# Optimization experiments

Measured on AMD Instinct MI355X. Metric: run time of the kernel, lower is better.

## Reference

```python
import jax, jax.numpy as jnp
import numpy as np

N, F_IN, HID, H1, NG = 50000, 128, 64, 4, 512
E = 800000


def setup_inputs() -> dict:
    key = jax.random.key(0)
    ks = jax.random.split(key, 16)
    x = jax.random.normal(ks[0], (N, F_IN), dtype=jnp.float32)
    edge_index = jax.random.randint(ks[1], (2, E), 0, N, dtype=jnp.int64)
    batch = jnp.sort(jax.random.randint(ks[2], (N,), 0, NG, dtype=jnp.int64))
    s = 0.05
    W1 = jax.random.normal(ks[3], (F_IN, H1 * HID), dtype=jnp.float32) * s
    a_src1 = jax.random.normal(ks[4], (H1, HID), dtype=jnp.float32) * s
    a_dst1 = jax.random.normal(ks[5], (H1, HID), dtype=jnp.float32) * s
    b1 = jnp.zeros((H1 * HID,), dtype=jnp.float32)
    W2 = jax.random.normal(ks[6], (H1 * HID, HID), dtype=jnp.float32) * s
    a_src2 = jax.random.normal(ks[7], (1, HID), dtype=jnp.float32) * s
    a_dst2 = jax.random.normal(ks[8], (1, HID), dtype=jnp.float32) * s
    b2 = jnp.zeros((HID,), dtype=jnp.float32)
    Wc = jax.random.normal(ks[9], (HID, 2), dtype=jnp.float32) * s
    bc = jnp.zeros((2,), dtype=jnp.float32)
    return dict(x=x, edge_index=edge_index, batch=batch, W1=W1, a_src1=a_src1,
                a_dst1=a_dst1, b1=b1, W2=W2, a_src2=a_src2, a_dst2=a_dst2,
                b2=b2, Wc=Wc, bc=bc)


def gat_layer(x, W, a_src, a_dst, bias, src, dst, n):
    # PyG GATConv: h = x @ W per head; e_ij = LeakyReLU(a_src.h_j + a_dst.h_i),
    # softmax over incoming edges of each dst node, then scatter-add aggregate.
    H, D = a_src.shape
    h = (x @ W).reshape(n, H, D)                       # [N,H,D]
    asrc = jnp.einsum('nhd,hd->nh', h, a_src)          # [N,H]
    adst = jnp.einsum('nhd,hd->nh', h, a_dst)
    e = jax.nn.leaky_relu(asrc[src] + adst[dst], 0.2)  # [E,H]
    m = jax.lax.stop_gradient(jax.ops.segment_max(e, dst, num_segments=n))
    p = jnp.exp(e - m[dst])
    s = jax.ops.segment_sum(p, dst, num_segments=n)
    alpha = p / (s[dst] + 1e-16)                       # [E,H]
    out = jax.ops.segment_sum(alpha[:, :, None] * h[src], dst, num_segments=n)
    return out.reshape(n, H * D) + bias


def reference(x, edge_index, batch, W1, a_src1, a_dst1, b1, W2, a_src2, a_dst2, b2, Wc, bc):
    n = x.shape[0]
    loops = jnp.arange(n, dtype=edge_index.dtype)
    src = jnp.concatenate([edge_index[0], loops])  # add self-loops (PyG default)
    dst = jnp.concatenate([edge_index[1], loops])
    h = jax.nn.relu(gat_layer(x, W1, a_src1, a_dst1, b1, src, dst, n))
    h = jax.nn.relu(gat_layer(h, W2, a_src2, a_dst2, b2, src, dst, n))
    # global mean pool over graphs
    ng = NG
    sums = jax.ops.segment_sum(h, batch, num_segments=ng)
    cnts = jax.ops.segment_sum(jnp.ones((n,), h.dtype), batch, num_segments=ng)
    pooled = sums / jnp.maximum(cnts, 1.0)[:, None]
    logits = pooled @ Wc + bc
    return jax.nn.log_softmax(logits, axis=1)
```

## Files before the change

kernel.cpp:

```cpp
#include <hip/hip_runtime.h>
#include <hip/hip_bf16.h>
#include <cstddef>
#include <cstdint>

#define FIN   128
#define HID   64
#define H1    4
#define NGRAPH 512
#define BCAP  8192

typedef short bf16x8 __attribute__((ext_vector_type(8)));
typedef float f32x4  __attribute__((ext_vector_type(4)));
typedef float f32x2  __attribute__((ext_vector_type(2)));

#if defined(__has_builtin)
#if __has_builtin(__builtin_amdgcn_cvt_f32_fp8) && __has_builtin(__builtin_amdgcn_cvt_pk_fp8_f32)
#define HAVE_HW_FP8 1
#endif
#if __has_builtin(__builtin_amdgcn_cvt_pk_f32_fp8)
#define HAVE_HW_FP8_PK 1
#endif
#endif

__device__ __forceinline__ float wave_reduce_sum(float v) {
  #pragma unroll
  for (int off = 32; off > 0; off >>= 1) v += __shfl_down(v, off, 64);
  return v;
}

__device__ __forceinline__ float leaky02(float x) {
  return x > 0.0f ? x : 0.2f * x;
}

__device__ __forceinline__ float bf2f(unsigned short u) {
  union { unsigned int i; float f; } v; v.i = ((unsigned int)u) << 16; return v.f;
}
__device__ __forceinline__ unsigned short f2bf(float f) {
  union { float f; unsigned int i; } v; v.f = f;
  unsigned int b = v.i;
  return (unsigned short)((b + 0x7FFFu + ((b >> 16) & 1u)) >> 16);
}

#ifndef HAVE_HW_FP8
__device__ __forceinline__ unsigned char f2fp8_1(float f) {
  unsigned int u = __float_as_uint(f);
  unsigned int s = u >> 31;
  u &= 0x7fffffffu;
  if (u > 0x43e00000u) u = 0x43e00000u;
  unsigned int b = u + (0x0007FFFFu + ((u >> 20) & 1u));
  int e = (int)(b >> 23) - 127;
  unsigned int m = (b >> 20) & 7u;
  unsigned char o;
  if (e < -9) o = 0;
  else if (e < -6) { int sh = -6 - e; o = (unsigned char)((8u | m) >> sh); }
  else if (e > 8) o = 0x7e;
  else o = (unsigned char)(((e + 7) << 3) | m);
  return o | (unsigned char)(s << 7);
}
#endif
__device__ __forceinline__ float fp8tof_1(unsigned char b) {
  unsigned int s = b >> 7, e = (b >> 3) & 15u, m = b & 7u;
  float v = (e == 0) ? (float)m * 0.001953125f
                     : (float)(8u + m) * __uint_as_float((117u + e) << 23);
  return s ? -v : v;
}

__device__ __forceinline__ unsigned char f2fp8(float f) {
#ifdef HAVE_HW_FP8
  return (unsigned char)(__builtin_amdgcn_cvt_pk_fp8_f32(f, f, 0u, false) & 0xffu);
#else
  return f2fp8_1(f);
#endif
}

__device__ __forceinline__ void fma4_fp8(unsigned int hw, float p,
                                         float& a0, float& a1, float& a2, float& a3) {
#ifdef HAVE_HW_FP8_PK
  f32x2 lo = __builtin_amdgcn_cvt_pk_f32_fp8((int)hw, false);
  f32x2 hi = __builtin_amdgcn_cvt_pk_f32_fp8((int)hw, true);
  a0 = fmaf(p, lo.x, a0);
  a1 = fmaf(p, lo.y, a1);
  a2 = fmaf(p, hi.x, a2);
  a3 = fmaf(p, hi.y, a3);
#elif defined(HAVE_HW_FP8)
  a0 = fmaf(p, __builtin_amdgcn_cvt_f32_fp8(hw, 0), a0);
  a1 = fmaf(p, __builtin_amdgcn_cvt_f32_fp8(hw, 1), a1);
  a2 = fmaf(p, __builtin_amdgcn_cvt_f32_fp8(hw, 2), a2);
  a3 = fmaf(p, __builtin_amdgcn_cvt_f32_fp8(hw, 3), a3);
#else
  a0 = fmaf(p, fp8tof_1((unsigned char)(hw & 0xffu)), a0);
  a1 = fmaf(p, fp8tof_1((unsigned char)((hw >> 8) & 0xffu)), a1);
  a2 = fmaf(p, fp8tof_1((unsigned char)((hw >> 16) & 0xffu)), a2);
  a3 = fmaf(p, fp8tof_1((unsigned char)((hw >> 24) & 0xffu)), a3);
#endif
}

#define P3K 8
__global__ __launch_bounds__(256)
void bpart_kernel(const int* __restrict__ src, const int* __restrict__ dst,
                  int* __restrict__ bucketFill, unsigned int* __restrict__ bucketBuf,
                  const float* __restrict__ W1, const float* __restrict__ W2,
                  unsigned short* __restrict__ W1T, unsigned short* __restrict__ W2T,
                  const int* __restrict__ batch, int* __restrict__ gstart,
                  int* __restrict__ gend, int E, int N, int nbuck) {
  int tid = threadIdx.x;
  int stride = gridDim.x * 256;
  int t0 = blockIdx.x * 256 + tid;
  for (int u = t0; u < 256 * 128; u += stride) {
    int n = u >> 7, k = u & 127;
    W1T[u] = f2bf(W1[(size_t)k * 256 + n]);
  }
  for (int u = t0; u < 64 * 256; u += stride) {
    int n = u >> 8, k = u & 255;
    W2T[u] = f2bf(W2[(size_t)k * 64 + n]);
  }
  for (int i = t0; i < N; i += stride) {
    int g = batch[i];
    if (i == 0 || batch[i - 1] != g) gstart[g] = i;
    if (i == N - 1 || batch[i + 1] != g) gend[g] = i + 1;
  }

  __shared__ int lhist[256];
  __shared__ int lbase[256];
  int chunk = 256 * P3K;
  for (int start = blockIdx.x * chunk; start < E; start += gridDim.x * chunk) {
    lhist[tid] = 0;
    __syncthreads();
    int mybuck[P3K]; unsigned int mypack[P3K]; int myrank[P3K];
    #pragma unroll
    for (int k = 0; k < P3K; k++) {
      int i = start + k * 256 + tid;
      if (i < E) {
        int d = dst[i];
        int b = d >> 8;
        mybuck[k] = b;
        mypack[k] = (unsigned int)src[i] | ((unsigned int)(d & 255) << 16);
        myrank[k] = atomicAdd(&lhist[b], 1);
      } else mybuck[k] = -1;
    }
    __syncthreads();
    if (tid < nbuck) lbase[tid] = (lhist[tid] > 0) ? atomicAdd(&bucketFill[tid], lhist[tid]) : 0;
    __syncthreads();
    #pragma unroll
    for (int k = 0; k < P3K; k++) {
      if (mybuck[k] >= 0) {
        int b = mybuck[k];
        int pos = lbase[b] + myrank[k];
        if (pos < BCAP) bucketBuf[((size_t)b << 13) + pos] = mypack[k];
      }
    }
    __syncthreads();
  }
}

__global__ __launch_bounds__(256)
void bbuild_gemm1_kernel(const unsigned int* __restrict__ bucketBuf,
                         const int* __restrict__ bucketFill,
                         int* __restrict__ rowstart, int* __restrict__ rowend,
                         unsigned short* __restrict__ csr,
                         const float* __restrict__ X, const unsigned short* __restrict__ W1T,
                         unsigned char* __restrict__ h1f8,
                         const float* __restrict__ a_src, const float* __restrict__ a_dst,
                         float* __restrict__ asv, float* __restrict__ adv,
                         int N, int nbuck) {
  __shared__ union {
    struct { unsigned short As[64][136]; unsigned short Bs[256][40]; } g;
    struct { int ldeg[256]; int lscan[256]; int lfill[256]; } b;
  } sm;
  int tid = threadIdx.x;

  if (blockIdx.x < (unsigned)nbuck) {
    int b = blockIdx.x;
    int r0 = b << 13;
    int cnt = bucketFill[b]; if (cnt > BCAP) cnt = BCAP;
    int nb0 = b << 8;
    sm.b.ldeg[tid] = 0;
    __syncthreads();
    for (int j = tid; j < cnt; j += 256)
      atomicAdd(&sm.b.ldeg[bucketBuf[r0 + j] >> 16], 1);
    __syncthreads();
    int v = sm.b.ldeg[tid];
    sm.b.lscan[tid] = v;
    __syncthreads();
    for (int off = 1; off < 256; off <<= 1) {
      int u = (tid >= off) ? sm.b.lscan[tid - off] : 0;
      __syncthreads();
      sm.b.lscan[tid] += u;
      __syncthreads();
    }
    int excl = sm.b.lscan[tid] - v;
    sm.b.lfill[tid] = excl;
    if (nb0 + tid < N) {
      rowstart[nb0 + tid] = r0 + excl;
      rowend[nb0 + tid]   = r0 + excl + v;
    }
    __syncthreads();
    for (int j = tid; j < cnt; j += 256) {
      unsigned int p = bucketBuf[r0 + j];
      int pos = r0 + atomicAdd(&sm.b.lfill[p >> 16], 1);
      csr[pos] = (unsigned short)(p & 0xffffu);
    }
    return;
  }

  int t = tid;
  int w = t >> 6, lane = t & 63;
  int quad = lane >> 4, l16 = lane & 15;
  int blockRow = (blockIdx.x - nbuck) * 64;

  {
    int node = t >> 2, kp = (t & 3) * 32;
    int gn = blockRow + node; if (gn >= N) gn = N - 1;
    const float4* xp = (const float4*)(X + (size_t)gn * 128 + kp);
    #pragma unroll
    for (int i = 0; i < 4; i++) {
      float4 va = xp[2 * i], vb = xp[2 * i + 1];
      union { unsigned short u[8]; uint4 v; } r;
      r.u[0] = f2bf(va.x); r.u[1] = f2bf(va.y); r.u[2] = f2bf(va.z); r.u[3] = f2bf(va.w);
      r.u[4] = f2bf(vb.x); r.u[5] = f2bf(vb.y); r.u[6] = f2bf(vb.z); r.u[7] = f2bf(vb.w);
      *(uint4*)&sm.g.As[node][kp + i * 8] = r.v;
    }
  }

  f32x4 acc[4][4];
  #pragma unroll
  for (int i = 0; i < 4; i++)
    #pragma unroll
    for (int j = 0; j < 4; j++) acc[i][j] = (f32x4){0.f, 0.f, 0.f, 0.f};

  for (int kc = 0; kc < FIN; kc += 32) {
    {
      const unsigned short* wp = W1T + (size_t)t * 128 + kc;
      #pragma unroll
      for (int i = 0; i < 4; i++) {
        uint4 v = *(const uint4*)(wp + i * 8);
        *(uint4*)&sm.g.Bs[t][i * 8] = v;
      }
    }
    __syncthreads();
    bf16x8 af[4], bfr[4];
    #pragma unroll
    for (int mt = 0; mt < 4; mt++)
      af[mt] = *(const bf16x8*)&sm.g.As[mt * 16 + l16][kc + quad * 8];
    #pragma unroll
    for (int nt = 0; nt < 4; nt++)
      bfr[nt] = *(const bf16x8*)&sm.g.Bs[w * 64 + nt * 16 + l16][quad * 8];
    #pragma unroll
    for (int mt = 0; mt < 4; mt++)
      #pragma unroll
      for (int nt = 0; nt < 4; nt++)
        acc[mt][nt] = __builtin_amdgcn_mfma_f32_16x16x32_bf16(af[mt], bfr[nt], acc[mt][nt], 0, 0, 0);
    __syncthreads();
  }

  float a_s[4], a_d[4];
  #pragma unroll
  for (int nt = 0; nt < 4; nt++) {
    a_s[nt] = a_src[w * 64 + nt * 16 + l16];
    a_d[nt] = a_dst[w * 64 + nt * 16 + l16];
  }
  #pragma unroll
  for (int mt = 0; mt < 4; mt++) {
    #pragma unroll
    for (int reg = 0; reg < 4; reg++) {
      int node = blockRow + mt * 16 + quad * 4 + reg;
      bool ok = node < N;
      float ps = 0.0f, pd = 0.0f;
      #pragma unroll
      for (int nt = 0; nt < 4; nt++) {
        float v = acc[mt][nt][reg];
        ps = fmaf(v, a_s[nt], ps);
        pd = fmaf(v, a_d[nt], pd);
        if (ok) h1f8[(size_t)node * 256 + w * 64 + nt * 16 + l16] = f2fp8(v);
      }
      #pragma unroll
      for (int off = 8; off > 0; off >>= 1) {
        ps += __shfl_xor(ps, off, 16);
        pd += __shfl_xor(pd, off, 16);
      }
      if (l16 == 0 && ok) {
        asv[(size_t)node * 4 + w] = ps;
        adv[(size_t)node * 4 + w] = pd;
      }
    }
  }
}

__global__ __launch_bounds__(256)
void gemm2_kernel(const unsigned short* __restrict__ out1b, const unsigned short* __restrict__ W2T,
                  unsigned char* __restrict__ h2f8,
                  const float* __restrict__ a_src, const float* __restrict__ a_dst,
                  float* __restrict__ asv, float* __restrict__ adv, int N) {
  __shared__ unsigned short As[64][40];
  __shared__ unsigned short Bs[64][40];
  int t = threadIdx.x;
  int w = t >> 6, lane = t & 63;
  int quad = lane >> 4, l16 = lane & 15;
  int blockRow = blockIdx.x * 64;

  f32x4 acc[4];
  #pragma unroll
  for (int j = 0; j < 4; j++) acc[j] = (f32x4){0.f, 0.f, 0.f, 0.f};

  int nodeS = t >> 2, koff = (t & 3) * 8;
  int gnS = blockRow + nodeS; if (gnS >= N) gnS = N - 1;

  for (int kc = 0; kc < 256; kc += 32) {
    {
      uint4 va = *(const uint4*)(out1b + (size_t)gnS * 256 + kc + koff);
      *(uint4*)&As[nodeS][koff] = va;
      uint4 vb = *(const uint4*)(W2T + (size_t)nodeS * 256 + kc + koff);
      *(uint4*)&Bs[nodeS][koff] = vb;
    }
    __syncthreads();
    bf16x8 af = *(const bf16x8*)&As[w * 16 + l16][quad * 8];
    #pragma unroll
    for (int nt = 0; nt < 4; nt++) {
      bf16x8 bfr = *(const bf16x8*)&Bs[nt * 16 + l16][quad * 8];
      acc[nt] = __builtin_amdgcn_mfma_f32_16x16x32_bf16(af, bfr, acc[nt], 0, 0, 0);
    }
    __syncthreads();
  }

  float a_s[4], a_d[4];
  #pragma unroll
  for (int nt = 0; nt < 4; nt++) {
    a_s[nt] = a_src[nt * 16 + l16];
    a_d[nt] = a_dst[nt * 16 + l16];
  }
  #pragma unroll
  for (int reg = 0; reg < 4; reg++) {
    int node = blockRow + w * 16 + quad * 4 + reg;
    bool ok = node < N;
    float ps = 0.0f, pd = 0.0f;
    #pragma unroll
    for (int nt = 0; nt < 4; nt++) {
      float v = acc[nt][reg];
      ps = fmaf(v, a_s[nt], ps);
      pd = fmaf(v, a_d[nt], pd);
      if (ok) h2f8[(size_t)node * 64 + nt * 16 + l16] = f2fp8(v);
    }
    #pragma unroll
    for (int off = 8; off > 0; off >>= 1) {
      ps += __shfl_xor(ps, off, 16);
      pd += __shfl_xor(pd, off, 16);
    }
    if (l16 == 0 && ok) { asv[node] = ps; adv[node] = pd; }
  }
}

__global__ __launch_bounds__(256)
void agg1_kernel(const unsigned char* __restrict__ h1f8, const int* __restrict__ rowstart,
                 const int* __restrict__ rowend, const unsigned short* __restrict__ csr,
                 const float* __restrict__ asv, const float* __restrict__ adv,
                 const float* __restrict__ b1, unsigned short* __restrict__ out1b, int N) {
  __shared__ int   sbuf[4][64];
  __shared__ float pbuf[4][4][68];
  int wv   = threadIdx.x >> 6;
  int lane = threadIdx.x & 63;
  int n = blockIdx.x * 4 + wv;
  if (n >= N) return;
  int r0 = rowstart[n], r1 = rowend[n];
  float4 ad = *(const float4*)(adv + (size_t)n * 4);
  float4 asn = *(const float4*)(asv + (size_t)n * 4);
  int hsel = lane >> 4;

  float es0 = leaky02(asn.x + ad.x);
  float es1 = leaky02(asn.y + ad.y);
  float es2 = leaky02(asn.z + ad.z);
  float es3 = leaky02(asn.w + ad.w);
  float esel = hsel == 0 ? es0 : (hsel == 1 ? es1 : (hsel == 2 ? es2 : es3));

  float ssum = 0.0f;
  float a0 = 0, a1 = 0, a2 = 0, a3 = 0;

  for (int base = r0; base < r1; base += 64) {
    int j = base + lane;
    int cnt = min(64, r1 - base);
    if (j < r1) {
      int s = csr[j];
      float4 as = *(const float4*)(asv + (size_t)s * 4);
      sbuf[wv][lane] = s;
      pbuf[wv][0][lane] = __expf(leaky02(as.x + ad.x));
      pbuf[wv][1][lane] = __expf(leaky02(as.y + ad.y));
      pbuf[wv][2][lane] = __expf(leaky02(as.z + ad.z));
      pbuf[wv][3][lane] = __expf(leaky02(as.w + ad.w));
    }
    __threadfence_block();

    int c = 0;
    for (; c + 8 <= cnt; c += 8) {
      int4 sv0 = *(const int4*)&sbuf[wv][c];
      int4 sv1 = *(const int4*)&sbuf[wv][c + 4];
      int sc0 = __builtin_amdgcn_readfirstlane(sv0.x);
      int sc1 = __builtin_amdgcn_readfirstlane(sv0.y);
      int sc2 = __builtin_amdgcn_readfirstlane(sv0.z);
      int sc3 = __builtin_amdgcn_readfirstlane(sv0.w);
      int sc4 = __builtin_amdgcn_readfirstlane(sv1.x);
      int sc5 = __builtin_amdgcn_readfirstlane(sv1.y);
      int sc6 = __builtin_amdgcn_readfirstlane(sv1.z);
      int sc7 = __builtin_amdgcn_readfirstlane(sv1.w);
      unsigned int hw0 = *((const unsigned int*)(h1f8 + ((size_t)sc0 << 8)) + lane);
      unsigned int hw1 = *((const unsigned int*)(h1f8 + ((size_t)sc1 << 8)) + lane);
      unsigned int hw2 = *((const unsigned int*)(h1f8 + ((size_t)sc2 << 8)) + lane);
      unsigned int hw3 = *((const unsigned int*)(h1f8 + ((size_t)sc3 << 8)) + lane);
      unsigned int hw4 = *((const unsigned int*)(h1f8 + ((size_t)sc4 << 8)) + lane);
      unsigned int hw5 = *((const unsigned int*)(h1f8 + ((size_t)sc5 << 8)) + lane);
      unsigned int hw6 = *((const unsigned int*)(h1f8 + ((size_t)sc6 << 8)) + lane);
      unsigned int hw7 = *((const unsigned int*)(h1f8 + ((size_t)sc7 << 8)) + lane);
      float4 pva = *(const float4*)&pbuf[wv][hsel][c];
      float4 pvb = *(const float4*)&pbuf[wv][hsel][c + 4];
      ssum += (pva.x + pva.y) + (pva.z + pva.w) + (pvb.x + pvb.y) + (pvb.z + pvb.w);
      fma4_fp8(hw0, pva.x, a0, a1, a2, a3);
      fma4_fp8(hw1, pva.y, a0, a1, a2, a3);
      fma4_fp8(hw2, pva.z, a0, a1, a2, a3);
      fma4_fp8(hw3, pva.w, a0, a1, a2, a3);
      fma4_fp8(hw4, pvb.x, a0, a1, a2, a3);
      fma4_fp8(hw5, pvb.y, a0, a1, a2, a3);
      fma4_fp8(hw6, pvb.z, a0, a1, a2, a3);
      fma4_fp8(hw7, pvb.w, a0, a1, a2, a3);
    }
    for (; c + 4 <= cnt; c += 4) {
      int4 sv = *(const int4*)&sbuf[wv][c];
      int sc0 = __builtin_amdgcn_readfirstlane(sv.x);
      int sc1 = __builtin_amdgcn_readfirstlane(sv.y);
      int sc2 = __builtin_amdgcn_readfirstlane(sv.z);
      int sc3 = __builtin_amdgcn_readfirstlane(sv.w);
      unsigned int hw0 = *((const unsigned int*)(h1f8 + ((size_t)sc0 << 8)) + lane);
      unsigned int hw1 = *((const unsigned int*)(h1f8 + ((size_t)sc1 << 8)) + lane);
      unsigned int hw2 = *((const unsigned int*)(h1f8 + ((size_t)sc2 << 8)) + lane);
      unsigned int hw3 = *((const unsigned int*)(h1f8 + ((size_t)sc3 << 8)) + lane);
      float4 pv = *(const float4*)&pbuf[wv][hsel][c];
      ssum += (pv.x + pv.y) + (pv.z + pv.w);
      fma4_fp8(hw0, pv.x, a0, a1, a2, a3);
      fma4_fp8(hw1, pv.y, a0, a1, a2, a3);
      fma4_fp8(hw2, pv.z, a0, a1, a2, a3);
      fma4_fp8(hw3, pv.w, a0, a1, a2, a3);
    }
    for (; c < cnt; c++) {
      int sc = __builtin_amdgcn_readfirstlane(sbuf[wv][c]);
      float psel = pbuf[wv][hsel][c];
      unsigned int hw = *((const unsigned int*)(h1f8 + ((size_t)sc << 8)) + lane);
      ssum += psel;
      fma4_fp8(hw, psel, a0, a1, a2, a3);
    }
    __threadfence_block();
  }

  {
    float psel = __expf(esel);
    ssum += psel;
    unsigned int hw = *((const unsigned int*)(h1f8 + ((size_t)n << 8)) + lane);
    fma4_fp8(hw, psel, a0, a1, a2, a3);
  }

  float inv = 1.0f / (ssum + 1e-16f);
  int d0 = lane * 4;
  float4 bv = *(const float4*)(b1 + d0);
  float v0 = a0 * inv + bv.x;
  float v1 = a1 * inv + bv.y;
  float v2 = a2 * inv + bv.z;
  float v3 = a3 * inv + bv.w;
  ushort4 o;
  o.x = f2bf(v0 > 0 ? v0 : 0.0f);
  o.y = f2bf(v1 > 0 ? v1 : 0.0f);
  o.z = f2bf(v2 > 0 ? v2 : 0.0f);
  o.w = f2bf(v3 > 0 ? v3 : 0.0f);
  *(ushort4*)(out1b + (size_t)n * 256 + d0) = o;
}

__global__ __launch_bounds__(256)
void agg2_kernel(const unsigned char* __restrict__ h2f8, const int* __restrict__ rowstart,
                 const int* __restrict__ rowend, const unsigned short* __restrict__ csr,
                 const float* __restrict__ asv, const float* __restrict__ adv,
                 const float* __restrict__ b2, unsigned short* __restrict__ h2b, int N) {
  __shared__ int   sbuf[4][64];
  __shared__ float pbuf[4][64];
  int wv   = threadIdx.x >> 6;
  int lane = threadIdx.x & 63;
  int quad = lane >> 4, l16 = lane & 15;
  int n = blockIdx.x * 4 + wv;
  if (n >= N) return;
  int r0 = rowstart[n], r1 = rowend[n];
  float ad = adv[n];
  float eself = leaky02(asv[n] + ad);
  float q = 0.0f;
  float a0 = 0, a1 = 0, a2 = 0, a3 = 0;

  for (int base = r0; base < r1; base += 64) {
    int j = base + lane;
    int cnt = min(64, r1 - base);
    if (j < r1) {
      int s = csr[j];
      sbuf[wv][lane] = s;
      pbuf[wv][lane] = __expf(leaky02(asv[s] + ad));
    }
    __threadfence_block();

    int c = 0;
    for (; c + 16 <= cnt; c += 16) {
      int scA = sbuf[wv][c + quad];
      int scB = sbuf[wv][c + 4 + quad];
      int scC = sbuf[wv][c + 8 + quad];
      int scD = sbuf[wv][c + 12 + quad];
      float pA = pbuf[wv][c + quad];
      float pB = pbuf[wv][c + 4 + quad];
      float pC = pbuf[wv][c + 8 + quad];
      float pD = pbuf[wv][c + 12 + quad];
      unsigned int hwA = *((const unsigned int*)(h2f8 + ((size_t)scA << 6)) + l16);
      unsigned int hwB = *((const unsigned int*)(h2f8 + ((size_t)scB << 6)) + l16);
      unsigned int hwC = *((const unsigned int*)(h2f8 + ((size_t)scC << 6)) + l16);
      unsigned int hwD = *((const unsigned int*)(h2f8 + ((size_t)scD << 6)) + l16);
      q += (pA + pB) + (pC + pD);
      fma4_fp8(hwA, pA, a0, a1, a2, a3);
      fma4_fp8(hwB, pB, a0, a1, a2, a3);
      fma4_fp8(hwC, pC, a0, a1, a2, a3);
      fma4_fp8(hwD, pD, a0, a1, a2, a3);
    }
    for (; c + 8 <= cnt; c += 8) {
      int scA = sbuf[wv][c + quad];
      int scB = sbuf[wv][c + 4 + quad];
      float pA = pbuf[wv][c + quad];
      float pB = pbuf[wv][c + 4 + quad];
      unsigned int hwA = *((const unsigned int*)(h2f8 + ((size_t)scA << 6)) + l16);
      unsigned int hwB = *((const unsigned int*)(h2f8 + ((size_t)scB << 6)) + l16);
      q += pA + pB;
      fma4_fp8(hwA, pA, a0, a1, a2, a3);
      fma4_fp8(hwB, pB, a0, a1, a2, a3);
    }
    for (; c + 4 <= cnt; c += 4) {
      int sc = sbuf[wv][c + quad];
      float p1 = pbuf[wv][c + quad];
      unsigned int hw = *((const unsigned int*)(h2f8 + ((size_t)sc << 6)) + l16);
      q += p1;
      fma4_fp8(hw, p1, a0, a1, a2, a3);
    }
    int rem = cnt - c;
    if (quad < rem) {
      int sc = sbuf[wv][c + quad];
      float p1 = pbuf[wv][c + quad];
      unsigned int hw = *((const unsigned int*)(h2f8 + ((size_t)sc << 6)) + l16);
      q += p1;
      fma4_fp8(hw, p1, a0, a1, a2, a3);
    }
    __threadfence_block();
  }

  #pragma unroll
  for (int off = 16; off <= 32; off <<= 1) {
    q  += __shfl_xor(q,  off, 64);
    a0 += __shfl_xor(a0, off, 64);
    a1 += __shfl_xor(a1, off, 64);
    a2 += __shfl_xor(a2, off, 64);
    a3 += __shfl_xor(a3, off, 64);
  }
  float ssum = q;

  {
    float p = __expf(eself);
    ssum += p;
    unsigned int hw = *((const unsigned int*)(h2f8 + ((size_t)n << 6)) + l16);
    fma4_fp8(hw, p, a0, a1, a2, a3);
  }

  if (quad == 0) {
    float inv = 1.0f / (ssum + 1e-16f);
    float4 bv = *(const float4*)(b2 + l16 * 4);
    float v0 = a0 * inv + bv.x;
    float v1 = a1 * inv + bv.y;
    float v2 = a2 * inv + bv.z;
    float v3 = a3 * inv + bv.w;
    ushort4 o;
    o.x = f2bf(v0 > 0 ? v0 : 0.0f);
    o.y = f2bf(v1 > 0 ? v1 : 0.0f);
    o.z = f2bf(v2 > 0 ? v2 : 0.0f);
    o.w = f2bf(v3 > 0 ? v3 : 0.0f);
    *(ushort4*)(h2b + (size_t)n * 64 + l16 * 4) = o;
  }
}

__global__ __launch_bounds__(256)
void pool_kernel(const unsigned short* __restrict__ h2b, const int* __restrict__ gstart,
                 const int* __restrict__ gend, const float* __restrict__ Wc,
                 const float* __restrict__ bc, float* __restrict__ out) {
  int g = blockIdx.x;
  int w = threadIdx.x >> 6, lane = threadIdx.x & 63;
  int s = gstart[g], e = gend[g];
  float acc = 0.0f;
  for (int n = s + w; n < e; n += 4) acc += bf2f(h2b[(size_t)n * 64 + lane]);
  __shared__ float red[4][64];
  red[w][lane] = acc;
  __syncthreads();
  if (w == 0) {
    float v = red[0][lane] + red[1][lane] + red[2][lane] + red[3][lane];
    float pooled = (e > s) ? v / (float)(e - s) : 0.0f;
    float l0 = wave_reduce_sum(pooled * Wc[lane * 2 + 0]);
    float l1 = wave_reduce_sum(pooled * Wc[lane * 2 + 1]);
    if (lane == 0) {
      l0 += bc[0]; l1 += bc[1];
      float mx = fmaxf(l0, l1);
      float lse = mx + logf(__expf(l0 - mx) + __expf(l1 - mx));
      out[g * 2 + 0] = l0 - lse;
      out[g * 2 + 1] = l1 - lse;
    }
  }
}

extern "C" void kernel_launch(void* const* d_in, const int* in_sizes, int n_in,
                              void* d_out, int out_size, void* d_ws, size_t ws_size,
                              hipStream_t stream) {
  const float* x      = (const float*)d_in[0];
  const int*   ei     = (const int*)d_in[1];
  const int*   batch  = (const int*)d_in[2];
  const float* W1     = (const float*)d_in[3];
  const float* a_src1 = (const float*)d_in[4];
  const float* a_dst1 = (const float*)d_in[5];
  const float* b1     = (const float*)d_in[6];
  const float* W2     = (const float*)d_in[7];
  const float* a_src2 = (const float*)d_in[8];
  const float* a_dst2 = (const float*)d_in[9];
  const float* b2     = (const float*)d_in[10];
  const float* Wc     = (const float*)d_in[11];
  const float* bc     = (const float*)d_in[12];
  float* out = (float*)d_out;

  const int N = in_sizes[0] / FIN;
  const int E = in_sizes[1] / 2;
  const int* srcArr = ei;
  const int* dstArr = ei + E;
  const int nbuck = (N + 255) >> 8;

  char* base = (char*)d_ws;
  size_t off = 0;
  auto alloc = [&](size_t bytes) -> void* {
    void* p = base + off;
    off = (off + bytes + 255) & ~(size_t)255;
    return p;
  };
  unsigned short* W1T  = (unsigned short*)alloc((size_t)256 * 128 * 2);
  unsigned short* W2T  = (unsigned short*)alloc((size_t)64 * 256 * 2);
  unsigned char*  h1f8 = (unsigned char*)alloc((size_t)N * 256);
  unsigned short* out1b= (unsigned short*)alloc((size_t)N * 256 * 2);
  unsigned char*  h2f8 = (unsigned char*)alloc((size_t)N * 64);
  unsigned short* h2b  = (unsigned short*)alloc((size_t)N * 64 * 2);
  float* asv1  = (float*)alloc((size_t)N * 4 * 4);
  float* adv1  = (float*)alloc((size_t)N * 4 * 4);
  float* asv2  = (float*)alloc((size_t)N * 4);
  float* adv2  = (float*)alloc((size_t)N * 4);
  int*   bucketFill= (int*)alloc(256 * 4);
  int*   gstart= (int*)alloc(NGRAPH * 4);
  int*   gend  = (int*)alloc(NGRAPH * 4);
  size_t zspan = (size_t)((char*)gend + NGRAPH * 4 - (char*)bucketFill);
  int*   rowstart = (int*)alloc((size_t)N * 4);
  int*   rowend   = (int*)alloc((size_t)N * 4);
  unsigned int* bucketBuf = (unsigned int*)alloc((size_t)nbuck * BCAP * 4);
  unsigned short* csr = (unsigned short*)alloc((size_t)nbuck * BCAP * 2);
  (void)ws_size; (void)n_in; (void)out_size;

  int gridWv = (N + 3) / 4;
  int gridG  = (N + 63) / 64;
  int gridP3 = (E + 256 * P3K - 1) / (256 * P3K);
  if (gridP3 > 1024) gridP3 = 1024;

  hipMemsetAsync(bucketFill, 0, zspan, stream);
  bpart_kernel<<<gridP3, 256, 0, stream>>>(srcArr, dstArr, bucketFill, bucketBuf,
                                           W1, W2, W1T, W2T, batch, gstart, gend,
                                           E, N, nbuck);
  bbuild_gemm1_kernel<<<nbuck + gridG, 256, 0, stream>>>(
      bucketBuf, bucketFill, rowstart, rowend, csr,
      x, W1T, h1f8, a_src1, a_dst1, asv1, adv1, N, nbuck);
  agg1_kernel<<<gridWv, 256, 0, stream>>>(h1f8, rowstart, rowend, csr, asv1, adv1, b1, out1b, N);

  gemm2_kernel<<<gridG, 256, 0, stream>>>(out1b, W2T, h2f8, a_src2, a_dst2, asv2, adv2, N);
  agg2_kernel<<<gridWv, 256, 0, stream>>>(h2f8, rowstart, rowend, csr, asv2, adv2, b2, h2b, N);

  pool_kernel<<<NGRAPH, 256, 0, stream>>>(h2b, gstart, gend, Wc, bc, out);
}
```

Before: 218.3 us.

## Fuse layer-1 aggregation with layer-2 GEMM via shared-memory staging

Merges the layer-1 aggregation and the layer-2 projection into one kernel. Each 512-thread block aggregates 8 nodes into shared memory as bf16, then one wave runs MFMA against W2T read from global memory and writes the fp8 h2 features and the attention scalars. This drops the out1b round trip through global memory and one kernel launch. In exchange, half of each 16-row MFMA tile is wasted, only one wave per block does the GEMM while the others wait, and W2T is re-read by every block.

```diff
diff --git a/kernel.cpp b/kernel.cpp
--- a/kernel.cpp
+++ b/kernel.cpp
@@ -286,187 +286,176 @@
   }
 }
 
-__global__ __launch_bounds__(256)
-void gemm2_kernel(const unsigned short* __restrict__ out1b, const unsigned short* __restrict__ W2T,
-                  unsigned char* __restrict__ h2f8,
-                  const float* __restrict__ a_src, const float* __restrict__ a_dst,
-                  float* __restrict__ asv, float* __restrict__ adv, int N) {
-  __shared__ unsigned short As[64][40];
-  __shared__ unsigned short Bs[64][40];
-  int t = threadIdx.x;
-  int w = t >> 6, lane = t & 63;
-  int quad = lane >> 4, l16 = lane & 15;
-  int blockRow = blockIdx.x * 64;
-
-  f32x4 acc[4];
-  #pragma unroll
-  for (int j = 0; j < 4; j++) acc[j] = (f32x4){0.f, 0.f, 0.f, 0.f};
-
-  int nodeS = t >> 2, koff = (t & 3) * 8;
-  int gnS = blockRow + nodeS; if (gnS >= N) gnS = N - 1;
-
-  for (int kc = 0; kc < 256; kc += 32) {
-    {
-      uint4 va = *(const uint4*)(out1b + (size_t)gnS * 256 + kc + koff);
-      *(uint4*)&As[nodeS][koff] = va;
-      uint4 vb = *(const uint4*)(W2T + (size_t)nodeS * 256 + kc + koff);
-      *(uint4*)&Bs[nodeS][koff] = vb;
-    }
-    __syncthreads();
-    bf16x8 af = *(const bf16x8*)&As[w * 16 + l16][quad * 8];
-    #pragma unroll
-    for (int nt = 0; nt < 4; nt++) {
-      bf16x8 bfr = *(const bf16x8*)&Bs[nt * 16 + l16][quad * 8];
-      acc[nt] = __builtin_amdgcn_mfma_f32_16x16x32_bf16(af, bfr, acc[nt], 0, 0, 0);
-    }
-    __syncthreads();
-  }
-
-  float a_s[4], a_d[4];
-  #pragma unroll
-  for (int nt = 0; nt < 4; nt++) {
-    a_s[nt] = a_src[nt * 16 + l16];
-    a_d[nt] = a_dst[nt * 16 + l16];
-  }
-  #pragma unroll
-  for (int reg = 0; reg < 4; reg++) {
-    int node = blockRow + w * 16 + quad * 4 + reg;
-    bool ok = node < N;
-    float ps = 0.0f, pd = 0.0f;
-    #pragma unroll
-    for (int nt = 0; nt < 4; nt++) {
-      float v = acc[nt][reg];
-      ps = fmaf(v, a_s[nt], ps);
-      pd = fmaf(v, a_d[nt], pd);
-      if (ok) h2f8[(size_t)node * 64 + nt * 16 + l16] = f2fp8(v);
-    }
-    #pragma unroll
-    for (int off = 8; off > 0; off >>= 1) {
-      ps += __shfl_xor(ps, off, 16);
-      pd += __shfl_xor(pd, off, 16);
-    }
-    if (l16 == 0 && ok) { asv[node] = ps; adv[node] = pd; }
-  }
-}
-
-__global__ __launch_bounds__(256)
-void agg1_kernel(const unsigned char* __restrict__ h1f8, const int* __restrict__ rowstart,
-                 const int* __restrict__ rowend, const unsigned short* __restrict__ csr,
-                 const float* __restrict__ asv, const float* __restrict__ adv,
-                 const float* __restrict__ b1, unsigned short* __restrict__ out1b, int N) {
-  __shared__ int   sbuf[4][64];
-  __shared__ float pbuf[4][4][68];
+__global__ __launch_bounds__(512, 4)
+void agg1g2_kernel(const unsigned char* __restrict__ h1f8, const int* __restrict__ rowstart,
+                   const int* __restrict__ rowend, const unsigned short* __restrict__ csr,
+                   const float* __restrict__ asv, const float* __restrict__ adv,
+                   const float* __restrict__ b1, const unsigned short* __restrict__ W2T,
+                   unsigned char* __restrict__ h2f8,
+                   const float* __restrict__ a_src2, const float* __restrict__ a_dst2,
+                   float* __restrict__ asv2, float* __restrict__ adv2, int N) {
+  __shared__ int   sbuf[8][64];
+  __shared__ float pbuf[8][4][68];
+  __shared__ unsigned short o1s[16][288];
   int wv   = threadIdx.x >> 6;
   int lane = threadIdx.x & 63;
-  int n = blockIdx.x * 4 + wv;
-  if (n >= N) return;
-  int r0 = rowstart[n], r1 = rowend[n];
-  float4 ad = *(const float4*)(adv + (size_t)n * 4);
-  float4 asn = *(const float4*)(asv + (size_t)n * 4);
-  int hsel = lane >> 4;
-
-  float es0 = leaky02(asn.x + ad.x);
-  float es1 = leaky02(asn.y + ad.y);
-  float es2 = leaky02(asn.z + ad.z);
-  float es3 = leaky02(asn.w + ad.w);
-  float esel = hsel == 0 ? es0 : (hsel == 1 ? es1 : (hsel == 2 ? es2 : es3));
-
-  float ssum = 0.0f;
-  float a0 = 0, a1 = 0, a2 = 0, a3 = 0;
-
-  for (int base = r0; base < r1; base += 64) {
-    int j = base + lane;
-    int cnt = min(64, r1 - base);
-    if (j < r1) {
-      int s = csr[j];
-      float4 as = *(const float4*)(asv + (size_t)s * 4);
-      sbuf[wv][lane] = s;
-      pbuf[wv][0][lane] = __expf(leaky02(as.x + ad.x));
-      pbuf[wv][1][lane] = __expf(leaky02(as.y + ad.y));
-      pbuf[wv][2][lane] = __expf(leaky02(as.z + ad.z));
-      pbuf[wv][3][lane] = __expf(leaky02(as.w + ad.w));
-    }
-    __threadfence_block();
-
-    int c = 0;
-    for (; c + 8 <= cnt; c += 8) {
-      int4 sv0 = *(const int4*)&sbuf[wv][c];
-      int4 sv1 = *(const int4*)&sbuf[wv][c + 4];
-      int sc0 = __builtin_amdgcn_readfirstlane(sv0.x);
-      int sc1 = __builtin_amdgcn_readfirstlane(sv0.y);
-      int sc2 = __builtin_amdgcn_readfirstlane(sv0.z);
-      int sc3 = __builtin_amdgcn_readfirstlane(sv0.w);
-      int sc4 = __builtin_amdgcn_readfirstlane(sv1.x);
-      int sc5 = __builtin_amdgcn_readfirstlane(sv1.y);
-      int sc6 = __builtin_amdgcn_readfirstlane(sv1.z);
-      int sc7 = __builtin_amdgcn_readfirstlane(sv1.w);
-      unsigned int hw0 = *((const unsigned int*)(h1f8 + ((size_t)sc0 << 8)) + lane);
-      unsigned int hw1 = *((const unsigned int*)(h1f8 + ((size_t)sc1 << 8)) + lane);
-      unsigned int hw2 = *((const unsigned int*)(h1f8 + ((size_t)sc2 << 8)) + lane);
-      unsigned int hw3 = *((const unsigned int*)(h1f8 + ((size_t)sc3 << 8)) + lane);
-      unsigned int hw4 = *((const unsigned int*)(h1f8 + ((size_t)sc4 << 8)) + lane);
-      unsigned int hw5 = *((const unsigned int*)(h1f8 + ((size_t)sc5 << 8)) + lane);
-      unsigned int hw6 = *((const unsigned int*)(h1f8 + ((size_t)sc6 << 8)) + lane);
-      unsigned int hw7 = *((const unsigned int*)(h1f8 + ((size_t)sc7 << 8)) + lane);
-      float4 pva = *(const float4*)&pbuf[wv][hsel][c];
-      float4 pvb = *(const float4*)&pbuf[wv][hsel][c + 4];
-      ssum += (pva.x + pva.y) + (pva.z + pva.w) + (pvb.x + pvb.y) + (pvb.z + pvb.w);
-      fma4_fp8(hw0, pva.x, a0, a1, a2, a3);
-      fma4_fp8(hw1, pva.y, a0, a1, a2, a3);
-      fma4_fp8(hw2, pva.z, a0, a1, a2, a3);
-      fma4_fp8(hw3, pva.w, a0, a1, a2, a3);
-      fma4_fp8(hw4, pvb.x, a0, a1, a2, a3);
-      fma4_fp8(hw5, pvb.y, a0, a1, a2, a3);
-      fma4_fp8(hw6, pvb.z, a0, a1, a2, a3);
-      fma4_fp8(hw7, pvb.w, a0, a1, a2, a3);
-    }
-    for (; c + 4 <= cnt; c += 4) {
-      int4 sv = *(const int4*)&sbuf[wv][c];
-      int sc0 = __builtin_amdgcn_readfirstlane(sv.x);
-      int sc1 = __builtin_amdgcn_readfirstlane(sv.y);
-      int sc2 = __builtin_amdgcn_readfirstlane(sv.z);
-      int sc3 = __builtin_amdgcn_readfirstlane(sv.w);
-      unsigned int hw0 = *((const unsigned int*)(h1f8 + ((size_t)sc0 << 8)) + lane);
-      unsigned int hw1 = *((const unsigned int*)(h1f8 + ((size_t)sc1 << 8)) + lane);
-      unsigned int hw2 = *((const unsigned int*)(h1f8 + ((size_t)sc2 << 8)) + lane);
-      unsigned int hw3 = *((const unsigned int*)(h1f8 + ((size_t)sc3 << 8)) + lane);
-      float4 pv = *(const float4*)&pbuf[wv][hsel][c];
-      ssum += (pv.x + pv.y) + (pv.z + pv.w);
-      fma4_fp8(hw0, pv.x, a0, a1, a2, a3);
-      fma4_fp8(hw1, pv.y, a0, a1, a2, a3);
-      fma4_fp8(hw2, pv.z, a0, a1, a2, a3);
-      fma4_fp8(hw3, pv.w, a0, a1, a2, a3);
-    }
-    for (; c < cnt; c++) {
-      int sc = __builtin_amdgcn_readfirstlane(sbuf[wv][c]);
-      float psel = pbuf[wv][hsel][c];
-      unsigned int hw = *((const unsigned int*)(h1f8 + ((size_t)sc << 8)) + lane);
+  int nb = blockIdx.x * 8;
+  int n = nb + wv;
+
+  if (n < N) {
+    int r0 = rowstart[n], r1 = rowend[n];
+    float4 ad = *(const float4*)(adv + (size_t)n * 4);
+    float4 asn = *(const float4*)(asv + (size_t)n * 4);
+    int hsel = lane >> 4;
+
+    float es0 = leaky02(asn.x + ad.x);
+    float es1 = leaky02(asn.y + ad.y);
+    float es2 = leaky02(asn.z + ad.z);
+    float es3 = leaky02(asn.w + ad.w);
+    float esel = hsel == 0 ? es0 : (hsel == 1 ? es1 : (hsel == 2 ? es2 : es3));
+
+    float ssum = 0.0f;
+    float a0 = 0, a1 = 0, a2 = 0, a3 = 0;
+
+    for (int base = r0; base < r1; base += 64) {
+      int j = base + lane;
+      int cnt = min(64, r1 - base);
+      if (j < r1) {
+        int s = csr[j];
+        float4 as = *(const float4*)(asv + (size_t)s * 4);
+        sbuf[wv][lane] = s;
+        pbuf[wv][0][lane] = __expf(leaky02(as.x + ad.x));
+        pbuf[wv][1][lane] = __expf(leaky02(as.y + ad.y));
+        pbuf[wv][2][lane] = __expf(leaky02(as.z + ad.z));
+        pbuf[wv][3][lane] = __expf(leaky02(as.w + ad.w));
+      }
+      __threadfence_block();
+
+      int c = 0;
+      for (; c + 8 <= cnt; c += 8) {
+        int4 sv0 = *(const int4*)&sbuf[wv][c];
+        int4 sv1 = *(const int4*)&sbuf[wv][c + 4];
+        int sc0 = __builtin_amdgcn_readfirstlane(sv0.x);
+        int sc1 = __builtin_amdgcn_readfirstlane(sv0.y);
+        int sc2 = __builtin_amdgcn_readfirstlane(sv0.z);
+        int sc3 = __builtin_amdgcn_readfirstlane(sv0.w);
+        int sc4 = __builtin_amdgcn_readfirstlane(sv1.x);
+        int sc5 = __builtin_amdgcn_readfirstlane(sv1.y);
+        int sc6 = __builtin_amdgcn_readfirstlane(sv1.z);
+        int sc7 = __builtin_amdgcn_readfirstlane(sv1.w);
+        unsigned int hw0 = *((const unsigned int*)(h1f8 + ((size_t)sc0 << 8)) + lane);
+        unsigned int hw1 = *((const unsigned int*)(h1f8 + ((size_t)sc1 << 8)) + lane);
+        unsigned int hw2 = *((const unsigned int*)(h1f8 + ((size_t)sc2 << 8)) + lane);
+        unsigned int hw3 = *((const unsigned int*)(h1f8 + ((size_t)sc3 << 8)) + lane);
+        unsigned int hw4 = *((const unsigned int*)(h1f8 + ((size_t)sc4 << 8)) + lane);
+        unsigned int hw5 = *((const unsigned int*)(h1f8 + ((size_t)sc5 << 8)) + lane);
+        unsigned int hw6 = *((const unsigned int*)(h1f8 + ((size_t)sc6 << 8)) + lane);
+        unsigned int hw7 = *((const unsigned int*)(h1f8 + ((size_t)sc7 << 8)) + lane);
+        float4 pva = *(const float4*)&pbuf[wv][hsel][c];
+        float4 pvb = *(const float4*)&pbuf[wv][hsel][c + 4];
+        ssum += (pva.x + pva.y) + (pva.z + pva.w) + (pvb.x + pvb.y) + (pvb.z + pvb.w);
+        fma4_fp8(hw0, pva.x, a0, a1, a2, a3);
+        fma4_fp8(hw1, pva.y, a0, a1, a2, a3);
+        fma4_fp8(hw2, pva.z, a0, a1, a2, a3);
+        fma4_fp8(hw3, pva.w, a0, a1, a2, a3);
+        fma4_fp8(hw4, pvb.x, a0, a1, a2, a3);
+        fma4_fp8(hw5, pvb.y, a0, a1, a2, a3);
+        fma4_fp8(hw6, pvb.z, a0, a1, a2, a3);
+        fma4_fp8(hw7, pvb.w, a0, a1, a2, a3);
+      }
+      for (; c + 4 <= cnt; c += 4) {
+        int4 sv = *(const int4*)&sbuf[wv][c];
+        int sc0 = __builtin_amdgcn_readfirstlane(sv.x);
+        int sc1 = __builtin_amdgcn_readfirstlane(sv.y);
+        int sc2 = __builtin_amdgcn_readfirstlane(sv.z);
+        int sc3 = __builtin_amdgcn_readfirstlane(sv.w);
+        unsigned int hw0 = *((const unsigned int*)(h1f8 + ((size_t)sc0 << 8)) + lane);
+        unsigned int hw1 = *((const unsigned int*)(h1f8 + ((size_t)sc1 << 8)) + lane);
+        unsigned int hw2 = *((const unsigned int*)(h1f8 + ((size_t)sc2 << 8)) + lane);
+        unsigned int hw3 = *((const unsigned int*)(h1f8 + ((size_t)sc3 << 8)) + lane);
+        float4 pv = *(const float4*)&pbuf[wv][hsel][c];
+        ssum += (pv.x + pv.y) + (pv.z + pv.w);
+        fma4_fp8(hw0, pv.x, a0, a1, a2, a3);
+        fma4_fp8(hw1, pv.y, a0, a1, a2, a3);
+        fma4_fp8(hw2, pv.z, a0, a1, a2, a3);
+        fma4_fp8(hw3, pv.w, a0, a1, a2, a3);
+      }
+      for (; c < cnt; c++) {
+        int sc = __builtin_amdgcn_readfirstlane(sbuf[wv][c]);
+        float psel = pbuf[wv][hsel][c];
+        unsigned int hw = *((const unsigned int*)(h1f8 + ((size_t)sc << 8)) + lane);
+        ssum += psel;
+        fma4_fp8(hw, psel, a0, a1, a2, a3);
+      }
+      __threadfence_block();
+    }
+
+    {
+      float psel = __expf(esel);
       ssum += psel;
+      unsigned int hw = *((const unsigned int*)(h1f8 + ((size_t)n << 8)) + lane);
       fma4_fp8(hw, psel, a0, a1, a2, a3);
     }
-    __threadfence_block();
-  }
-
-  {
-    float psel = __expf(esel);
-    ssum += psel;
-    unsigned int hw = *((const unsigned int*)(h1f8 + ((size_t)n << 8)) + lane);
-    fma4_fp8(hw, psel, a0, a1, a2, a3);
-  }
-
-  float inv = 1.0f / (ssum + 1e-16f);
-  int d0 = lane * 4;
-  float4 bv = *(const float4*)(b1 + d0);
-  float v0 = a0 * inv + bv.x;
-  float v1 = a1 * inv + bv.y;
-  float v2 = a2 * inv + bv.z;
-  float v3 = a3 * inv + bv.w;
-  ushort4 o;
-  o.x = f2bf(v0 > 0 ? v0 : 0.0f);
-  o.y = f2bf(v1 > 0 ? v1 : 0.0f);
-  o.z = f2bf(v2 > 0 ? v2 : 0.0f);
-  o.w = f2bf(v3 > 0 ? v3 : 0.0f);
-  *(ushort4*)(out1b + (size_t)n * 256 + d0) = o;
+
+    float inv = 1.0f / (ssum + 1e-16f);
+    int d0 = lane * 4;
+    float4 bv = *(const float4*)(b1 + d0);
+    float v0 = a0 * inv + bv.x;
+    float v1 = a1 * inv + bv.y;
+    float v2 = a2 * inv + bv.z;
+    float v3 = a3 * inv + bv.w;
+    ushort4 o;
+    o.x = f2bf(v0 > 0 ? v0 : 0.0f);
+    o.y = f2bf(v1 > 0 ? v1 : 0.0f);
+    o.z = f2bf(v2 > 0 ? v2 : 0.0f);
+    o.w = f2bf(v3 > 0 ? v3 : 0.0f);
+    *(ushort4*)&o1s[wv][d0] = o;
+  }
+
+  __syncthreads();
+
+  if (threadIdx.x < 64) {
+    int quad = lane >> 4, l16 = lane & 15;
+    f32x4 acc[4];
+    #pragma unroll
+    for (int j = 0; j < 4; j++) acc[j] = (f32x4){0.f, 0.f, 0.f, 0.f};
+
+    for (int kc = 0; kc < 256; kc += 32) {
+      bf16x8 af = *(const bf16x8*)&o1s[l16][kc + quad * 8];
+      #pragma unroll
+      for (int nt = 0; nt < 4; nt++) {
+        bf16x8 bfr = *(const bf16x8*)(W2T + (size_t)(nt * 16 + l16) * 256 + kc + quad * 8);
+        acc[nt] = __builtin_amdgcn_mfma_f32_16x16x32_bf16(af, bfr, acc[nt], 0, 0, 0);
+      }
+    }
+
+    float a_s[4], a_d[4];
+    #pragma unroll
+    for (int nt = 0; nt < 4; nt++) {
+      a_s[nt] = a_src2[nt * 16 + l16];
+      a_d[nt] = a_dst2[nt * 16 + l16];
+    }
+    #pragma unroll
+    for (int reg = 0; reg < 4; reg++) {
+      int rq = quad * 4 + reg;
+      int node = nb + rq;
+      bool ok = (rq < 8) && (node < N);
+      float ps = 0.0f, pd = 0.0f;
+      #pragma unroll
+      for (int nt = 0; nt < 4; nt++) {
+        float v = acc[nt][reg];
+        ps = fmaf(v, a_s[nt], ps);
+        pd = fmaf(v, a_d[nt], pd);
+        if (ok) h2f8[(size_t)node * 64 + nt * 16 + l16] = f2fp8(v);
+      }
+      #pragma unroll
+      for (int off = 8; off > 0; off >>= 1) {
+        ps += __shfl_xor(ps, off, 16);
+        pd += __shfl_xor(pd, off, 16);
+      }
+      if (l16 == 0 && ok) { asv2[node] = ps; adv2[node] = pd; }
+    }
+  }
 }
 
 __global__ __launch_bounds__(256)
@@ -640,7 +629,6 @@
   unsigned short* W1T  = (unsigned short*)alloc((size_t)256 * 128 * 2);
   unsigned short* W2T  = (unsigned short*)alloc((size_t)64 * 256 * 2);
   unsigned char*  h1f8 = (unsigned char*)alloc((size_t)N * 256);
-  unsigned short* out1b= (unsigned short*)alloc((size_t)N * 256 * 2);
   unsigned char*  h2f8 = (unsigned char*)alloc((size_t)N * 64);
   unsigned short* h2b  = (unsigned short*)alloc((size_t)N * 64 * 2);
   float* asv1  = (float*)alloc((size_t)N * 4 * 4);
@@ -659,6 +647,7 @@
 
   int gridWv = (N + 3) / 4;
   int gridG  = (N + 63) / 64;
+  int gridF  = (N + 7) / 8;
   int gridP3 = (E + 256 * P3K - 1) / (256 * P3K);
   if (gridP3 > 1024) gridP3 = 1024;
 
@@ -669,9 +658,11 @@
   bbuild_gemm1_kernel<<<nbuck + gridG, 256, 0, stream>>>(
       bucketBuf, bucketFill, rowstart, rowend, csr,
       x, W1T, h1f8, a_src1, a_dst1, asv1, adv1, N, nbuck);
-  agg1_kernel<<<gridWv, 256, 0, stream>>>(h1f8, rowstart, rowend, csr, asv1, adv1, b1, out1b, N);
-
-  gemm2_kernel<<<gridG, 256, 0, stream>>>(out1b, W2T, h2f8, a_src2, a_dst2, asv2, adv2, N);
+
+  agg1g2_kernel<<<gridF, 512, 0, stream>>>(h1f8, rowstart, rowend, csr, asv1, adv1,
+                                           b1, W2T, h2f8, a_src2, a_dst2,
+                                           asv2, adv2, N);
+
   agg2_kernel<<<gridWv, 256, 0, stream>>>(h2f8, rowstart, rowend, csr, asv2, adv2, b2, h2b, N);
 
   pool_kernel<<<NGRAPH, 256, 0, stream>>>(h2b, gstart, gend, Wc, bc, out);
```

Measured after the change: 227.7 us. 1.04x slower.
